# Kernel tuning notes

Measured on AMD Instinct MI355X. Metric: run time of the kernel, lower is better.

Reference implementation:

```python
import jax, jax.numpy as jnp
import numpy as np
import math


def _alibi_slopes(num_heads: int) -> np.ndarray:
    def power_of_2(n):
        ratio = 2.0 ** (-8.0 / n)
        return np.array([ratio ** i for i in range(n)], dtype=np.float32)
    if math.log2(num_heads).is_integer():
        return power_of_2(num_heads)
    nearest = 2 ** math.floor(math.log2(num_heads))
    return np.concatenate([power_of_2(nearest), power_of_2(2 * nearest)[::2][: num_heads - nearest]])


def _rmsnorm(x, w, eps=1e-6):
    var = jnp.mean(x * x, axis=-1, keepdims=True)
    return x * jax.lax.rsqrt(var + eps) * w


def setup_inputs() -> dict:
    key = jax.random.key(0)
    ks = jax.random.split(key, 6)
    B, S, M = 2, 2048, 1024
    H, KV, D = 16, 4, 64
    s = 0.02
    return {
        "features": jax.random.normal(ks[0], (B, S, M), jnp.float32),
        "wq": jax.random.normal(ks[1], (H * D, M), jnp.float32) * s,
        "wk": jax.random.normal(ks[2], (KV * D, M), jnp.float32) * s,
        "wv": jax.random.normal(ks[3], (KV * D, M), jnp.float32) * s,
        "wo": jax.random.normal(ks[4], (M, H * D), jnp.float32) * s,
        "q_norm_w": jnp.ones((H * D,), jnp.float32),
        "k_norm_w": jnp.ones((KV * D,), jnp.float32),
        "num_heads": 16,
        "num_kv_heads": 4,
        "head_dim": 64,
        "sliding_window": 512,
    }


def reference(features, wq, wk, wv, wo, q_norm_w, k_norm_w, num_heads, num_kv_heads, head_dim, sliding_window):
    B, S, M = features.shape
    H, KV, D = num_heads, num_kv_heads, head_dim
    kv_rep = H // KV

    q = features @ wq.T                                   # [B,S,H*D]
    k = features @ wk.T                                   # [B,S,KV*D]
    v = features @ wv.T                                   # [B,S,KV*D]
    q = _rmsnorm(q, q_norm_w)
    k = _rmsnorm(k, k_norm_w)

    q = q.reshape(B, S, H, D).transpose(0, 2, 1, 3)       # [B,H,S,D]
    k = k.reshape(B, S, KV, D)
    v = v.reshape(B, S, KV, D)
    k = jnp.repeat(k, kv_rep, axis=2).transpose(0, 2, 1, 3)  # [B,H,S,D]
    v = jnp.repeat(v, kv_rep, axis=2).transpose(0, 2, 1, 3)

    pos = jnp.arange(S)
    rel = pos[None, :] - pos[:, None]                     # [S,S], j - i
    slopes = jnp.asarray(_alibi_slopes(H))
    bias = slopes[:, None, None] * rel.astype(features.dtype)  # [H,S,S]
    invalid = (rel > 0) | (rel < -sliding_window)         # causal + left window
    bias = jnp.where(invalid[None], -jnp.inf, bias)

    scores = jnp.einsum("bhqd,bhkd->bhqk", q, k) / math.sqrt(D)
    attn = jax.nn.softmax(scores + bias[None], axis=-1)
    out = jnp.einsum("bhqk,bhkd->bhqd", attn, v)
    out = out.transpose(0, 2, 1, 3).reshape(B, S, H * D)
    return out @ wo.T
```

## Files before the change

### kernel.cpp

```cpp
#include <hip/hip_runtime.h>
#include <hip/hip_bf16.h>

typedef __bf16 bf16_t;
typedef bf16_t bf16x8 __attribute__((ext_vector_type(8)));
typedef bf16_t bf16x4 __attribute__((ext_vector_type(4)));
typedef float  f32x4  __attribute__((ext_vector_type(4)));
typedef float  f32x16 __attribute__((ext_vector_type(16)));

__device__ __forceinline__ f32x4 mfma16(bf16x8 a, bf16x8 b, f32x4 c) {
  return __builtin_amdgcn_mfma_f32_16x16x32_bf16(a, b, c, 0, 0, 0);
}
__device__ __forceinline__ f32x16 mfma32(bf16x8 a, bf16x8 b, f32x16 c) {
  return __builtin_amdgcn_mfma_f32_32x32x16_bf16(a, b, c, 0, 0, 0);
}

__global__ __launch_bounds__(256) void cast_all_k(const float* __restrict__ f,
                                                  const float* __restrict__ wq,
                                                  const float* __restrict__ wk,
                                                  const float* __restrict__ wv,
                                                  const float* __restrict__ wo,
                                                  bf16_t* __restrict__ Xbf,
                                                  bf16_t* __restrict__ Wqkv,
                                                  bf16_t* __restrict__ Wo) {
  int i = blockIdx.x * 256 + threadIdx.x;
  const float* src; bf16_t* dst; int off;
  if (i < 1048576)      { src = f;  dst = Xbf;                 off = 0; }
  else if (i < 1310720) { src = wq; dst = Wqkv;                off = 1048576; }
  else if (i < 1376256) { src = wk; dst = Wqkv + 1024 * 1024;  off = 1310720; }
  else if (i < 1441792) { src = wv; dst = Wqkv + 1280 * 1024;  off = 1376256; }
  else if (i < 1703936) { src = wo; dst = Wo;                  off = 1441792; }
  else return;
  int j = i - off;
  float4 v = reinterpret_cast<const float4*>(src)[j];
  bf16x4 o = { (bf16_t)v.x, (bf16_t)v.y, (bf16_t)v.z, (bf16_t)v.w };
  reinterpret_cast<bf16x4*>(dst)[j] = o;
}

__global__ __launch_bounds__(256) void gemm_bt(const bf16_t* __restrict__ A,
                                               const bf16_t* __restrict__ B,
                                               float* __restrict__ C,
                                               int M, int N, int K) {
  __shared__ __align__(16) unsigned short sA[2][128 * 64];
  __shared__ __align__(16) unsigned short sB[2][128 * 64];
  const int tid = threadIdx.x;
  const int lane = tid & 63;
  const int wid = tid >> 6;
  const int wm = wid >> 1, wn = wid & 1;
  const int lr = lane & 15, lg = lane >> 4;
  const int m0 = blockIdx.y * 128, n0 = blockIdx.x * 128;

  f32x4 acc[4][4] = {};

  auto STAGE = [&](int buf, int k0) {
#pragma unroll
    for (int r = 0; r < 4; ++r) {
      int e = r * 2048 + tid * 8;
      int row = e >> 6;
      int c = ((e >> 3) & 7) ^ (row & 7);
      const bf16_t* ga = A + (size_t)(m0 + row) * K + k0 + c * 8;
      __builtin_amdgcn_global_load_lds(
          (const __attribute__((address_space(1))) void*)ga,
          (__attribute__((address_space(3))) void*)(&sA[buf][r * 2048 + wid * 512]), 16, 0, 0);
      const bf16_t* gb = B + (size_t)(n0 + row) * K + k0 + c * 8;
      __builtin_amdgcn_global_load_lds(
          (const __attribute__((address_space(1))) void*)gb,
          (__attribute__((address_space(3))) void*)(&sB[buf][r * 2048 + wid * 512]), 16, 0, 0);
    }
  };

  const int nt = K >> 6;
  STAGE(0, 0);
  __syncthreads();
  int cur = 0;
  for (int t = 0; t < nt; ++t) {
    if (t + 1 < nt) STAGE(cur ^ 1, (t + 1) << 6);
#pragma unroll
    for (int ks = 0; ks < 2; ++ks) {
      bf16x8 afr[4], bfr[4];
#pragma unroll
      for (int m = 0; m < 4; ++m) {
        int row = wm * 64 + m * 16 + lr;
        int sc = (ks * 4 + lg) ^ (row & 7);
        afr[m] = *reinterpret_cast<const bf16x8*>(&sA[cur][row * 64 + sc * 8]);
      }
#pragma unroll
      for (int n = 0; n < 4; ++n) {
        int row = wn * 64 + n * 16 + lr;
        int sc = (ks * 4 + lg) ^ (row & 7);
        bfr[n] = *reinterpret_cast<const bf16x8*>(&sB[cur][row * 64 + sc * 8]);
      }
#pragma unroll
      for (int m = 0; m < 4; ++m)
#pragma unroll
        for (int n = 0; n < 4; ++n)
          acc[m][n] = mfma16(afr[m], bfr[n], acc[m][n]);
    }
    __syncthreads();
    cur ^= 1;
  }
#pragma unroll
  for (int m = 0; m < 4; ++m)
#pragma unroll
    for (int n = 0; n < 4; ++n) {
      int row = m0 + wm * 64 + m * 16 + lg * 4;
      int col = n0 + wn * 64 + n * 16 + lr;
#pragma unroll
      for (int r2 = 0; r2 < 4; ++r2)
        C[(size_t)(row + r2) * N + col] = acc[m][n][r2];
    }
}

__global__ __launch_bounds__(256) void rmsnorm_k(const float* __restrict__ qkv,
                                                 const float* __restrict__ qw,
                                                 const float* __restrict__ kw,
                                                 bf16_t* __restrict__ qn,
                                                 bf16_t* __restrict__ kn) {
  const int row = blockIdx.x;
  const int b = row >> 11, s = row & 2047;
  const int tid = threadIdx.x;
  const float* rp = qkv + (size_t)row * 1536;
  float4 q4 = *reinterpret_cast<const float4*>(rp + tid * 4);
  float kv1 = rp[1024 + tid];
  float sq = q4.x * q4.x + q4.y * q4.y + q4.z * q4.z + q4.w * q4.w;
  float sk = kv1 * kv1;
#pragma unroll
  for (int d = 1; d < 64; d <<= 1) {
    sq += __shfl_xor(sq, d, 64);
    sk += __shfl_xor(sk, d, 64);
  }
  __shared__ float red[2][4];
  if ((tid & 63) == 0) { red[0][tid >> 6] = sq; red[1][tid >> 6] = sk; }
  __syncthreads();
  sq = red[0][0] + red[0][1] + red[0][2] + red[0][3];
  sk = red[1][0] + red[1][1] + red[1][2] + red[1][3];
  const float rq = rsqrtf(sq * (1.0f / 1024.0f) + 1e-6f);
  const float rk = rsqrtf(sk * (1.0f / 256.0f) + 1e-6f);
  float4 w4 = *reinterpret_cast<const float4*>(qw + tid * 4);
  const int c = tid * 4, hh = c >> 6, d0 = c & 63;
  bf16x4 o = { (bf16_t)(q4.x * rq * w4.x), (bf16_t)(q4.y * rq * w4.y),
               (bf16_t)(q4.z * rq * w4.z), (bf16_t)(q4.w * rq * w4.w) };
  *reinterpret_cast<bf16x4*>(qn + ((size_t)((b * 16 + hh) * 2048 + s)) * 64 + d0) = o;
  const int kvh = tid >> 6, dk = tid & 63;
  kn[((size_t)((b * 4 + kvh) * 2048 + s)) * 64 + dk] = (bf16_t)(kv1 * rk * kw[tid]);
}

__global__ __launch_bounds__(256) void transpose_v_k(const float* __restrict__ qkv,
                                                     bf16_t* __restrict__ vt) {
  __shared__ float t[64][65];
  const int s0 = blockIdx.x * 64;
  const int bkv = blockIdx.y;
  const int b = bkv >> 2, kv = bkv & 3;
  const int tid = threadIdx.x;
  const int r = tid >> 2, cg = (tid & 3) * 16;
  const float* src = qkv + (size_t)(b * 2048 + s0 + r) * 1536 + 1280 + kv * 64 + cg;
#pragma unroll
  for (int j = 0; j < 4; ++j) {
    float4 v = *reinterpret_cast<const float4*>(src + j * 4);
    t[r][cg + j * 4 + 0] = v.x; t[r][cg + j * 4 + 1] = v.y;
    t[r][cg + j * 4 + 2] = v.z; t[r][cg + j * 4 + 3] = v.w;
  }
  __syncthreads();
  const int dl = tid >> 4;
  const int sl = (tid & 15) * 4;
  const int kt = (s0 >> 5) + (sl >> 5);
  const int kk = sl & 31;
#pragma unroll
  for (int p = 0; p < 4; ++p) {
    const int d = dl + p * 16;
    bf16x4 o = { (bf16_t)t[sl + 0][d], (bf16_t)t[sl + 1][d],
                 (bf16_t)t[sl + 2][d], (bf16_t)t[sl + 3][d] };
    *reinterpret_cast<bf16x4*>(vt + (size_t)bkv * 131072 + (size_t)kt * 2048 + d * 32 + kk) = o;
  }
}

__global__ __launch_bounds__(256, 4) void attn_k(const bf16_t* __restrict__ qn,
                                                 const bf16_t* __restrict__ kn,
                                                 const bf16_t* __restrict__ vt,
                                                 bf16_t* __restrict__ ao) {
  constexpr int S = 2048, D = 64, H = 16, KV = 4, WIN = 512;
  const int bkv = blockIdx.x;
  const int b = bkv >> 2, kv = bkv & 3;
  const int h = kv * 4 + blockIdx.z;
  const int wid = threadIdx.x >> 6;
  const int pair = wid >> 1;
  const int kh = wid & 1;
  const int qblk = blockIdx.y * 2 + pair;
  const int lane = threadIdx.x & 63;
  const int c = lane & 31;
  const int hi = lane >> 5;
  const int qbase = qblk * 32;
  const int q = qbase + c;

  __shared__ float mls[2][2][2][32];
  __shared__ float accbuf[2][64][33];

  const bf16_t* qp = qn + ((size_t)(b * H + h) * S + q) * D + hi * 8;
  bf16x8 qf[4];
#pragma unroll
  for (int cd = 0; cd < 4; ++cd) qf[cd] = *reinterpret_cast<const bf16x8*>(qp + cd * 16);

  const bf16_t* kb = kn + (size_t)bkv * S * D;
  const bf16_t* vb = vt + (size_t)bkv * 131072;

  const float L2E = 1.4426950408889634f;
  const float c1 = L2E / 8.0f;
  const float c2 = exp2f(-0.5f * (float)h) * L2E;

  f32x16 acc0 = {}, acc1 = {};
  float m_run = -3.0e38f, l_run = 0.0f;

  const int ktTop = qbase >> 5;
  const int kt0 = (qbase >= WIN) ? ((qbase - WIN) >> 5) : 0;

  for (int kt = ktTop - kh; kt >= kt0; kt -= 2) {
    const int k0 = kt << 5;
    const bf16_t* kp = kb + (((size_t)k0 + c) << 6) + hi * 8;
    f32x16 sfa = {};
#pragma unroll
    for (int cd = 0; cd < 4; ++cd) {
      bf16x8 kf = *reinterpret_cast<const bf16x8*>(kp + cd * 16);
      sfa = mfma32(kf, qf[cd], sfa);
    }
    const bool mtop = (kt == ktTop);
    const bool mbot = (k0 + WIN < qbase + 32);
    float t[16];
    float pmax = -3.0e38f;
    if (mtop | mbot) {
#pragma unroll
      for (int r = 0; r < 16; ++r) {
        const int kk = k0 + (r & 3) + 8 * (r >> 2) + 4 * hi;
        const int rel = kk - q;
        float tv = sfa[r] * c1 + c2 * (float)rel;
        if (rel > 0 || rel < -WIN) tv = -3.0e38f;
        t[r] = tv;
        pmax = fmaxf(pmax, tv);
      }
    } else {
      const float bb = c2 * (float)(k0 + 4 * hi - q);
#pragma unroll
      for (int r = 0; r < 16; ++r) {
        const float koff = (float)((r & 3) + 8 * (r >> 2));
        float tv = fmaf(sfa[r], c1, fmaf(koff, c2, bb));
        t[r] = tv;
        pmax = fmaxf(pmax, tv);
      }
    }
    pmax = fmaxf(pmax, __shfl_xor(pmax, 32, 64));
    if (!__all(pmax <= m_run + 8.0f)) {
      const float mnew = fmaxf(m_run, pmax);
      const float sc = exp2f(m_run - mnew);
      m_run = mnew;
      l_run *= sc;
#pragma unroll
      for (int r = 0; r < 16; ++r) {
        const int qi = (r & 3) + 8 * (r >> 2) + 4 * hi;
        const float scr = __shfl(sc, qi, 64);
        acc0[r] *= scr;
        acc1[r] *= scr;
      }
    }
    float rs = 0.0f;
    unsigned w[8];
#pragma unroll
    for (int i = 0; i < 8; ++i) {
      float e0 = exp2f(t[2 * i] - m_run);
      float e1 = exp2f(t[2 * i + 1] - m_run);
      rs += e0 + e1;
      union { bf16_t hh[2]; unsigned u; } pk;
      pk.hh[0] = (bf16_t)e0; pk.hh[1] = (bf16_t)e1;
      w[i] = pk.u;
    }
    rs += __shfl_xor(rs, 32, 64);
    l_run += rs;
    unsigned s0 = __shfl_xor(w[0], 32, 64), s1 = __shfl_xor(w[1], 32, 64);
    unsigned s2 = __shfl_xor(w[2], 32, 64), s3 = __shfl_xor(w[3], 32, 64);
    unsigned s4 = __shfl_xor(w[4], 32, 64), s5 = __shfl_xor(w[5], 32, 64);
    unsigned s6 = __shfl_xor(w[6], 32, 64), s7 = __shfl_xor(w[7], 32, 64);
    union { unsigned u[4]; bf16x8 v; } pa0, pa1;
    if (hi == 0) {
      pa0.u[0] = w[0]; pa0.u[1] = w[1]; pa0.u[2] = s0; pa0.u[3] = s1;
      pa1.u[0] = w[4]; pa1.u[1] = w[5]; pa1.u[2] = s4; pa1.u[3] = s5;
    } else {
      pa0.u[0] = s2; pa0.u[1] = s3; pa0.u[2] = w[2]; pa0.u[3] = w[3];
      pa1.u[0] = s6; pa1.u[1] = s7; pa1.u[2] = w[6]; pa1.u[3] = w[7];
    }
    const bf16_t* vp = vb + ((size_t)kt << 11) + c * 32 + hi * 8;
    bf16x8 v00 = *reinterpret_cast<const bf16x8*>(vp);
    bf16x8 v01 = *reinterpret_cast<const bf16x8*>(vp + 16);
    bf16x8 v10 = *reinterpret_cast<const bf16x8*>(vp + 1024);
    bf16x8 v11 = *reinterpret_cast<const bf16x8*>(vp + 1024 + 16);
    acc0 = mfma32(pa0.v, v00, acc0);
    acc0 = mfma32(pa1.v, v01, acc0);
    acc1 = mfma32(pa0.v, v10, acc1);
    acc1 = mfma32(pa1.v, v11, acc1);
  }

  mls[pair][kh][0][c] = m_run;
  mls[pair][kh][1][c] = l_run;
  __syncthreads();
  const float mo = mls[pair][kh ^ 1][0][c];
  const float lo = mls[pair][kh ^ 1][1][c];
  const float mt = fmaxf(m_run, mo);
  const float sc_self = exp2f(m_run - mt);
#pragma unroll
  for (int r = 0; r < 16; ++r) {
    const int qi = (r & 3) + 8 * (r >> 2) + 4 * hi;
    const float scr = __shfl(sc_self, qi, 64);
    acc0[r] *= scr;
    acc1[r] *= scr;
  }
  if (kh == 1) {
#pragma unroll
    for (int r = 0; r < 16; ++r) {
      accbuf[pair][lane][r] = acc0[r];
      accbuf[pair][lane][r + 16] = acc1[r];
    }
  }
  __syncthreads();
  if (kh == 0) {
    const float l_tot = l_run * sc_self + lo * exp2f(mo - mt);
#pragma unroll
    for (int r = 0; r < 16; ++r) {
      acc0[r] += accbuf[pair][lane][r];
      acc1[r] += accbuf[pair][lane][r + 16];
    }
#pragma unroll
    for (int r = 0; r < 16; ++r) {
      const int qi = (r & 3) + 8 * (r >> 2) + 4 * hi;
      const float lr = __shfl(l_tot, qi, 64);
      const float inv = 1.0f / lr;
      bf16_t* op = ao + ((size_t)(b * S + qbase + qi)) * 1024 + h * 64 + c;
      op[0]  = (bf16_t)(acc0[r] * inv);
      op[32] = (bf16_t)(acc1[r] * inv);
    }
  }
}

extern "C" void kernel_launch(void* const* d_in, const int* in_sizes, int n_in,
                              void* d_out, int out_size, void* d_ws, size_t ws_size,
                              hipStream_t stream) {
  const float* features = (const float*)d_in[0];
  const float* wq = (const float*)d_in[1];
  const float* wk = (const float*)d_in[2];
  const float* wv = (const float*)d_in[3];
  const float* wo = (const float*)d_in[4];
  const float* qw = (const float*)d_in[5];
  const float* kw = (const float*)d_in[6];
  float* out = (float*)d_out;

  bf16_t* Xbf  = (bf16_t*)d_ws;
  bf16_t* Wqkv = Xbf + 4096 * 1024;
  bf16_t* Wo   = Wqkv + 1536 * 1024;
  float*  QKVr = (float*)(Wo + 1024 * 1024);
  bf16_t* Qn   = (bf16_t*)(QKVr + 4096 * 1536);
  bf16_t* Kn   = Qn + 2 * 16 * 2048 * 64;
  bf16_t* Vt   = Kn + 2 * 4 * 2048 * 64;
  bf16_t* Ao   = Vt + 2 * 4 * 64 * 2048;

  cast_all_k<<<6656, 256, 0, stream>>>(features, wq, wk, wv, wo, Xbf, Wqkv, Wo);
  gemm_bt<<<dim3(12, 32), 256, 0, stream>>>(Xbf, Wqkv, QKVr, 4096, 1536, 1024);
  rmsnorm_k<<<4096, 256, 0, stream>>>(QKVr, qw, kw, Qn, Kn);
  transpose_v_k<<<dim3(32, 8), 256, 0, stream>>>(QKVr, Vt);
  attn_k<<<dim3(8, 32, 4), 256, 0, stream>>>(Qn, Kn, Vt, Ao);
  gemm_bt<<<dim3(8, 32), 256, 0, stream>>>(Ao, Wo, out, 4096, 1024, 1024);
}
```

Measured before the change: 97.69 us.

## Use fixed softmax max bound in attention and smaller GEMM M-tiles

The attention kernel drops the online running max and rescaling. It subtracts a fixed constant bound, which relies on RMS-normalised q and k keeping scores small, and this also removes the cross-wave max merge at the end. The GEMM is templated on its M tile, and both projections now launch with 64-row tiles, doubling the block count so more of the device is busy. s_setprio hints are placed around the MFMA groups. The fixed bound could lose accuracy or overflow if the scores grow larger than assumed, for example with non-unit norm weights.

```diff
diff --git a/kernel.cpp b/kernel.cpp
--- a/kernel.cpp
+++ b/kernel.cpp
@@ -36,32 +36,40 @@
   reinterpret_cast<bf16x4*>(dst)[j] = o;
 }
 
+template<int BM>
 __global__ __launch_bounds__(256) void gemm_bt(const bf16_t* __restrict__ A,
                                                const bf16_t* __restrict__ B,
                                                float* __restrict__ C,
                                                int M, int N, int K) {
-  __shared__ __align__(16) unsigned short sA[2][128 * 64];
+  constexpr int MR = BM / 32;
+  __shared__ __align__(16) unsigned short sA[2][BM * 64];
   __shared__ __align__(16) unsigned short sB[2][128 * 64];
   const int tid = threadIdx.x;
   const int lane = tid & 63;
   const int wid = tid >> 6;
   const int wm = wid >> 1, wn = wid & 1;
   const int lr = lane & 15, lg = lane >> 4;
-  const int m0 = blockIdx.y * 128, n0 = blockIdx.x * 128;
-
-  f32x4 acc[4][4] = {};
+  const int m0 = blockIdx.y * BM, n0 = blockIdx.x * 128;
+
+  f32x4 acc[MR][4] = {};
 
   auto STAGE = [&](int buf, int k0) {
+#pragma unroll
+    for (int r = 0; r < BM / 32; ++r) {
+      int e = r * 2048 + tid * 8;
+      int row = e >> 6;
+      int cc = ((e >> 3) & 7) ^ (row & 7);
+      const bf16_t* ga = A + (size_t)(m0 + row) * K + k0 + cc * 8;
+      __builtin_amdgcn_global_load_lds(
+          (const __attribute__((address_space(1))) void*)ga,
+          (__attribute__((address_space(3))) void*)(&sA[buf][r * 2048 + wid * 512]), 16, 0, 0);
+    }
 #pragma unroll
     for (int r = 0; r < 4; ++r) {
       int e = r * 2048 + tid * 8;
       int row = e >> 6;
-      int c = ((e >> 3) & 7) ^ (row & 7);
-      const bf16_t* ga = A + (size_t)(m0 + row) * K + k0 + c * 8;
-      __builtin_amdgcn_global_load_lds(
-          (const __attribute__((address_space(1))) void*)ga,
-          (__attribute__((address_space(3))) void*)(&sA[buf][r * 2048 + wid * 512]), 16, 0, 0);
-      const bf16_t* gb = B + (size_t)(n0 + row) * K + k0 + c * 8;
+      int cc = ((e >> 3) & 7) ^ (row & 7);
+      const bf16_t* gb = B + (size_t)(n0 + row) * K + k0 + cc * 8;
       __builtin_amdgcn_global_load_lds(
           (const __attribute__((address_space(1))) void*)gb,
           (__attribute__((address_space(3))) void*)(&sB[buf][r * 2048 + wid * 512]), 16, 0, 0);
@@ -76,10 +84,10 @@
     if (t + 1 < nt) STAGE(cur ^ 1, (t + 1) << 6);
 #pragma unroll
     for (int ks = 0; ks < 2; ++ks) {
-      bf16x8 afr[4], bfr[4];
-#pragma unroll
-      for (int m = 0; m < 4; ++m) {
-        int row = wm * 64 + m * 16 + lr;
+      bf16x8 afr[MR], bfr[4];
+#pragma unroll
+      for (int m = 0; m < MR; ++m) {
+        int row = wm * (BM / 2) + m * 16 + lr;
         int sc = (ks * 4 + lg) ^ (row & 7);
         afr[m] = *reinterpret_cast<const bf16x8*>(&sA[cur][row * 64 + sc * 8]);
       }
@@ -90,7 +98,7 @@
         bfr[n] = *reinterpret_cast<const bf16x8*>(&sB[cur][row * 64 + sc * 8]);
       }
 #pragma unroll
-      for (int m = 0; m < 4; ++m)
+      for (int m = 0; m < MR; ++m)
 #pragma unroll
         for (int n = 0; n < 4; ++n)
           acc[m][n] = mfma16(afr[m], bfr[n], acc[m][n]);
@@ -99,10 +107,10 @@
     cur ^= 1;
   }
 #pragma unroll
-  for (int m = 0; m < 4; ++m)
+  for (int m = 0; m < MR; ++m)
 #pragma unroll
     for (int n = 0; n < 4; ++n) {
-      int row = m0 + wm * 64 + m * 16 + lg * 4;
+      int row = m0 + wm * (BM / 2) + m * 16 + lg * 4;
       int col = n0 + wn * 64 + n * 16 + lr;
 #pragma unroll
       for (int r2 = 0; r2 < 4; ++r2)
@@ -191,7 +199,7 @@
   const int qbase = qblk * 32;
   const int q = qbase + c;
 
-  __shared__ float mls[2][2][2][32];
+  __shared__ float lsh[2][2][32];
   __shared__ float accbuf[2][64][33];
 
   const bf16_t* qp = qn + ((size_t)(b * H + h) * S + q) * D + hi * 8;
@@ -203,11 +211,12 @@
   const bf16_t* vb = vt + (size_t)bkv * 131072;
 
   const float L2E = 1.4426950408889634f;
+  const float MSTAT = 8.0f * L2E;
   const float c1 = L2E / 8.0f;
   const float c2 = exp2f(-0.5f * (float)h) * L2E;
 
   f32x16 acc0 = {}, acc1 = {};
-  float m_run = -3.0e38f, l_run = 0.0f;
+  float l_run = 0.0f;
 
   const int ktTop = qbase >> 5;
   const int kt0 = (qbase >= WIN) ? ((qbase - WIN) >> 5) : 0;
@@ -216,58 +225,36 @@
     const int k0 = kt << 5;
     const bf16_t* kp = kb + (((size_t)k0 + c) << 6) + hi * 8;
     f32x16 sfa = {};
+    __builtin_amdgcn_s_setprio(1);
 #pragma unroll
     for (int cd = 0; cd < 4; ++cd) {
       bf16x8 kf = *reinterpret_cast<const bf16x8*>(kp + cd * 16);
       sfa = mfma32(kf, qf[cd], sfa);
     }
-    const bool mtop = (kt == ktTop);
-    const bool mbot = (k0 + WIN < qbase + 32);
-    float t[16];
-    float pmax = -3.0e38f;
-    if (mtop | mbot) {
-#pragma unroll
-      for (int r = 0; r < 16; ++r) {
-        const int kk = k0 + (r & 3) + 8 * (r >> 2) + 4 * hi;
-        const int rel = kk - q;
-        float tv = sfa[r] * c1 + c2 * (float)rel;
-        if (rel > 0 || rel < -WIN) tv = -3.0e38f;
-        t[r] = tv;
-        pmax = fmaxf(pmax, tv);
-      }
-    } else {
-      const float bb = c2 * (float)(k0 + 4 * hi - q);
-#pragma unroll
-      for (int r = 0; r < 16; ++r) {
-        const float koff = (float)((r & 3) + 8 * (r >> 2));
-        float tv = fmaf(sfa[r], c1, fmaf(koff, c2, bb));
-        t[r] = tv;
-        pmax = fmaxf(pmax, tv);
-      }
-    }
-    pmax = fmaxf(pmax, __shfl_xor(pmax, 32, 64));
-    if (!__all(pmax <= m_run + 8.0f)) {
-      const float mnew = fmaxf(m_run, pmax);
-      const float sc = exp2f(m_run - mnew);
-      m_run = mnew;
-      l_run *= sc;
-#pragma unroll
-      for (int r = 0; r < 16; ++r) {
-        const int qi = (r & 3) + 8 * (r >> 2) + 4 * hi;
-        const float scr = __shfl(sc, qi, 64);
-        acc0[r] *= scr;
-        acc1[r] *= scr;
-      }
-    }
+    __builtin_amdgcn_s_setprio(0);
+    const bool edge = (kt == ktTop) | (k0 + WIN < qbase + 32);
+    const float bbm = fmaf(c2, (float)(k0 + 4 * hi - q), -MSTAT);
     float rs = 0.0f;
     unsigned w[8];
 #pragma unroll
     for (int i = 0; i < 8; ++i) {
-      float e0 = exp2f(t[2 * i] - m_run);
-      float e1 = exp2f(t[2 * i + 1] - m_run);
-      rs += e0 + e1;
+      float e2[2];
+#pragma unroll
+      for (int j = 0; j < 2; ++j) {
+        const int r = 2 * i + j;
+        const float koff = (float)((r & 3) + 8 * (r >> 2));
+        if (edge) {
+          const int rel = k0 + (int)koff + 4 * hi - q;
+          float tv = fmaf(sfa[r], c1, fmaf((float)rel, c2, -MSTAT));
+          tv = (rel > 0 || rel < -WIN) ? -3.0e38f : tv;
+          e2[j] = exp2f(tv);
+        } else {
+          e2[j] = exp2f(fmaf(sfa[r], c1, fmaf(koff, c2, bbm)));
+        }
+      }
+      rs += e2[0] + e2[1];
       union { bf16_t hh[2]; unsigned u; } pk;
-      pk.hh[0] = (bf16_t)e0; pk.hh[1] = (bf16_t)e1;
+      pk.hh[0] = (bf16_t)e2[0]; pk.hh[1] = (bf16_t)e2[1];
       w[i] = pk.u;
     }
     rs += __shfl_xor(rs, 32, 64);
@@ -289,26 +276,15 @@
     bf16x8 v01 = *reinterpret_cast<const bf16x8*>(vp + 16);
     bf16x8 v10 = *reinterpret_cast<const bf16x8*>(vp + 1024);
     bf16x8 v11 = *reinterpret_cast<const bf16x8*>(vp + 1024 + 16);
+    __builtin_amdgcn_s_setprio(1);
     acc0 = mfma32(pa0.v, v00, acc0);
     acc0 = mfma32(pa1.v, v01, acc0);
     acc1 = mfma32(pa0.v, v10, acc1);
     acc1 = mfma32(pa1.v, v11, acc1);
-  }
-
-  mls[pair][kh][0][c] = m_run;
-  mls[pair][kh][1][c] = l_run;
-  __syncthreads();
-  const float mo = mls[pair][kh ^ 1][0][c];
-  const float lo = mls[pair][kh ^ 1][1][c];
-  const float mt = fmaxf(m_run, mo);
-  const float sc_self = exp2f(m_run - mt);
-#pragma unroll
-  for (int r = 0; r < 16; ++r) {
-    const int qi = (r & 3) + 8 * (r >> 2) + 4 * hi;
-    const float scr = __shfl(sc_self, qi, 64);
-    acc0[r] *= scr;
-    acc1[r] *= scr;
-  }
+    __builtin_amdgcn_s_setprio(0);
+  }
+
+  lsh[pair][kh][c] = l_run;
   if (kh == 1) {
 #pragma unroll
     for (int r = 0; r < 16; ++r) {
@@ -318,7 +294,7 @@
   }
   __syncthreads();
   if (kh == 0) {
-    const float l_tot = l_run * sc_self + lo * exp2f(mo - mt);
+    const float l_tot = l_run + lsh[pair][1][c];
 #pragma unroll
     for (int r = 0; r < 16; ++r) {
       acc0[r] += accbuf[pair][lane][r];
@@ -358,9 +334,9 @@
   bf16_t* Ao   = Vt + 2 * 4 * 64 * 2048;
 
   cast_all_k<<<6656, 256, 0, stream>>>(features, wq, wk, wv, wo, Xbf, Wqkv, Wo);
-  gemm_bt<<<dim3(12, 32), 256, 0, stream>>>(Xbf, Wqkv, QKVr, 4096, 1536, 1024);
+  gemm_bt<64><<<dim3(12, 64), 256, 0, stream>>>(Xbf, Wqkv, QKVr, 4096, 1536, 1024);
   rmsnorm_k<<<4096, 256, 0, stream>>>(QKVr, qw, kw, Qn, Kn);
   transpose_v_k<<<dim3(32, 8), 256, 0, stream>>>(QKVr, Vt);
   attn_k<<<dim3(8, 32, 4), 256, 0, stream>>>(Qn, Kn, Vt, Ao);
-  gemm_bt<<<dim3(8, 32), 256, 0, stream>>>(Ao, Wo, out, 4096, 1024, 1024);
-}
+  gemm_bt<64><<<dim3(8, 64), 256, 0, stream>>>(Ao, Wo, out, 4096, 1024, 1024);
+}
```

After: 93.05 us. 4.8% less time.
